# Optimization experiments

Measured on AMD Instinct MI355X. Metric: run time of the kernel, lower is better.

The kernel has to match this reference:

```python
import jax, jax.numpy as jnp
import numpy as np

N = 100000      # nodes per graph batch
E = 1600000     # edges
G = 64          # graphs (segments for GraphNorm)
F_IN = 128
F = 128         # hidden features
H = 4           # attention heads
C = F // H      # per-head channels
F_OUT = 64
N_GAT = 2       # layers - 2
EPS = 1e-5


def _add_self_loops(src, dst, n):
    loop = jnp.arange(n, dtype=src.dtype)
    return jnp.concatenate([src, loop]), jnp.concatenate([dst, loop])


def gcn_conv(x, src, dst, W, b, n):
    # PyG GCNConv: self-loops + symmetric deg^-1/2 normalization, add-aggr
    src, dst = _add_self_loops(src, dst, n)
    deg = jax.ops.segment_sum(jnp.ones(src.shape, x.dtype), dst, num_segments=n)
    dis = jnp.where(deg > 0, jax.lax.rsqrt(deg), 0.0)
    norm = dis[src] * dis[dst]                      # [E+N]
    h = x @ W.T                                     # [N,F]
    return jax.ops.segment_sum(h[src] * norm[:, None], dst, num_segments=n) + b


def graph_norm(x, batch, gamma, beta, alpha, g):
    # PyG GraphNorm: x_c = x - alpha*mean_g; out = gamma*x_c/sqrt(var_g+eps)+beta
    cnt = jnp.maximum(jax.ops.segment_sum(jnp.ones((x.shape[0],), x.dtype), batch, num_segments=g), 1.0)[:, None]
    mean = jax.ops.segment_sum(x, batch, num_segments=g) / cnt
    xc = x - alpha * mean[batch]
    var = jax.ops.segment_sum(xc * xc, batch, num_segments=g) / cnt
    return gamma * xc / jnp.sqrt(var[batch] + EPS) + beta


def gat_conv(x, src, dst, W, att_src, att_dst, b, n):
    # PyG GATConv (shared src/dst lin, self-loops, LeakyReLU(0.2), segment softmax)
    h = (x @ W.T).reshape(n, H, C)                  # [N,H,C]
    a_s = (h * att_src).sum(-1)                     # [N,H]
    a_d = (h * att_dst).sum(-1)                     # [N,H]
    src, dst = _add_self_loops(src, dst, n)
    e = jax.nn.leaky_relu(a_s[src] + a_d[dst], 0.2) # [E+N,H]
    emax = jax.ops.segment_max(e, dst, num_segments=n)
    ex = jnp.exp(e - emax[dst])
    den = jax.ops.segment_sum(ex, dst, num_segments=n)
    alpha = ex / (den[dst] + 1e-16)                 # [E+N,H]
    out = jax.ops.segment_sum(h[src] * alpha[:, :, None], dst, num_segments=n)
    return out.reshape(n, H * C) + b


def _branch(x, src, dst, batch, W0, b0, gn0_gamma, gn0_beta, gn0_alpha,
            gat_W, gat_att_src, gat_att_dst, gat_b, gn_gamma, gn_beta, gn_alpha,
            lin_W, lin_b):
    x = gcn_conv(x, src, dst, W0, b0, N)
    x = graph_norm(x, batch, gn0_gamma, gn0_beta, gn0_alpha, G)
    for i in range(N_GAT):
        h = gat_conv(x, src, dst, gat_W[i], gat_att_src[i], gat_att_dst[i], gat_b[i], N)
        h = jax.nn.gelu(h, approximate=False)
        x = x + graph_norm(h, batch, gn_gamma[i], gn_beta[i], gn_alpha[i], G)
    return x @ lin_W.T + lin_b


def setup_inputs() -> dict:
    key = jax.random.key(0)
    ks = jax.random.split(key, 16)
    inp = {
        'x1': jax.random.normal(ks[0], (N, F_IN), jnp.float32),
        'x2': jax.random.normal(ks[1], (N, F_IN), jnp.float32),
        'edge_index1': jax.random.randint(ks[2], (2, E), 0, N, jnp.int32),
        'edge_index2': jax.random.randint(ks[3], (2, E), 0, N, jnp.int32),
        'batch1': jnp.sort(jax.random.randint(ks[4], (N,), 0, G, jnp.int32)),
        'batch2': jnp.sort(jax.random.randint(ks[5], (N,), 0, G, jnp.int32)),
        'W0': jax.random.normal(ks[6], (F, F_IN), jnp.float32) * 0.05,
        'b0': jnp.zeros((F,), jnp.float32),
        'gn0_gamma': jnp.ones((F,), jnp.float32),
        'gn0_beta': jnp.zeros((F,), jnp.float32),
        'gn0_alpha': jnp.ones((F,), jnp.float32),
        'gat_W': jax.random.normal(ks[7], (N_GAT, F, F), jnp.float32) * 0.05,
        'gat_att_src': jax.random.normal(ks[8], (N_GAT, H, C), jnp.float32) * 0.05,
        'gat_att_dst': jax.random.normal(ks[9], (N_GAT, H, C), jnp.float32) * 0.05,
        'gat_b': jnp.zeros((N_GAT, F), jnp.float32),
        'gn_gamma': jnp.ones((N_GAT, F), jnp.float32),
        'gn_beta': jnp.zeros((N_GAT, F), jnp.float32),
        'gn_alpha': jnp.ones((N_GAT, F), jnp.float32),
        'lin_W': jax.random.normal(ks[10], (F_OUT, F), jnp.float32) * 0.05,
        'lin_b': jnp.zeros((F_OUT,), jnp.float32),
    }
    return inp


def reference(x1, x2, edge_index1, edge_index2, batch1, batch2,
              W0, b0, gn0_gamma, gn0_beta, gn0_alpha,
              gat_W, gat_att_src, gat_att_dst, gat_b, gn_gamma, gn_beta, gn_alpha,
              lin_W, lin_b):
    params = (W0, b0, gn0_gamma, gn0_beta, gn0_alpha, gat_W, gat_att_src,
              gat_att_dst, gat_b, gn_gamma, gn_beta, gn_alpha, lin_W, lin_b)
    o1 = _branch(x1, edge_index1[0], edge_index1[1], batch1, *params)
    o2 = _branch(x2, edge_index2[0], edge_index2[1], batch2, *params)
    return jnp.stack([o1, o2])  # [2, N, F_OUT]
```

## Files before the change

### kernel.cpp

```cpp
#include <hip/hip_runtime.h>
#include <hip/hip_bf16.h>

#define NN 100000
#define EE 1600000
#define GB 64

typedef unsigned int u32;
typedef unsigned short u16;

typedef __attribute__((ext_vector_type(8))) short bf16x8;
typedef __attribute__((ext_vector_type(4))) float f32x4;

#define CDIV(a, b) (((a) + (b) - 1) / (b))
#define NSB CDIV(NN, 1024)
#define NBB CDIV(EE, 4096)

__device__ __forceinline__ float bf2f(u16 v) { return __uint_as_float(((u32)v) << 16); }
__device__ __forceinline__ u16 f2bf(float f) {
    u32 u = __float_as_uint(f);
    u32 r = (u + 0x7fffu + ((u >> 16) & 1u)) >> 16;
    return (u16)r;
}
__device__ __forceinline__ float lrelu(float v) { return fmaxf(v, 0.2f * v); }
__device__ __forceinline__ float gelu_f(float v) { return 0.5f * v * (1.f + erff(v * 0.70710678118654752f)); }
__device__ __forceinline__ float cexp(float v) { return __expf(fminf(v, 30.f)); }

__global__ __launch_bounds__(256) void k_zero_f(float* __restrict__ p, int n) {
    int i = blockIdx.x * 256 + threadIdx.x;
    if (i < n) p[i] = 0.f;
}
__global__ __launch_bounds__(256) void k_zero_i(int* __restrict__ p, int n) {
    int i = blockIdx.x * 256 + threadIdx.x;
    if (i < n) p[i] = 0;
}
__global__ __launch_bounds__(256) void k_f2bf_arr(const float* __restrict__ src, u16* __restrict__ dst, int n) {
    int i4 = (blockIdx.x * 256 + threadIdx.x) * 4;
    if (i4 >= n) return;
    float4 v = *(const float4*)(src + i4);
    *(ushort4*)(dst + i4) = make_ushort4(f2bf(v.x), f2bf(v.y), f2bf(v.z), f2bf(v.w));
}

__global__ void k_cnt2(const int* __restrict__ b0, const int* __restrict__ b1, float* __restrict__ cnt, int n) {
    int t = threadIdx.x;
    if (t >= 128) return;
    int graph = t >> 6, g = t & 63;
    const int* batch = graph ? b1 : b0;
    int lo = 0, hi = n;
    while (lo < hi) { int m = (lo + hi) >> 1; if (batch[m] <= g) lo = m + 1; else hi = m; }
    int ub_g = lo;
    int v = g - 1;
    lo = 0; hi = n;
    while (lo < hi) { int m = (lo + hi) >> 1; if (batch[m] <= v) lo = m + 1; else hi = m; }
    cnt[graph * GB + g] = (float)(ub_g - lo);
}

__global__ __launch_bounds__(256) void k_bincnt(const int* __restrict__ d0, const int* __restrict__ d1,
                                                int* __restrict__ bin_cnt) {
    __shared__ int lcnt[NSB];
    int g = blockIdx.x / NBB, blk = blockIdx.x % NBB;
    const int* dst = g ? d1 : d0;
    int t = threadIdx.x;
    for (int i = t; i < NSB; i += 256) lcnt[i] = 0;
    __syncthreads();
    int base = blk * 4096;
#pragma unroll
    for (int k = 0; k < 16; ++k) {
        int ei = base + k * 256 + t;
        if (ei < EE) {
            int d = dst[ei];
            if ((u32)d < (u32)NN) atomicAdd(&lcnt[d >> 10], 1);
        }
    }
    __syncthreads();
    for (int i = t; i < NSB; i += 256)
        if (lcnt[i]) atomicAdd(&bin_cnt[g * NSB + i], lcnt[i]);
}

__global__ __launch_bounds__(128) void k_binscan(const int* __restrict__ bin_cnt, int* __restrict__ bin_base,
                                                 int* __restrict__ bin_cur, int* __restrict__ ptr) {
    __shared__ int sh[128];
    int g = blockIdx.x;
    int t = threadIdx.x;
    int v = (t < NSB) ? bin_cnt[g * NSB + t] : 0;
    sh[t] = v;
    __syncthreads();
    for (int o = 1; o < 128; o <<= 1) {
        int x = (t >= o) ? sh[t - o] : 0;
        __syncthreads();
        sh[t] += x;
        __syncthreads();
    }
    if (t < NSB) {
        bin_base[g * (NSB + 1) + t] = sh[t] - v;
        bin_cur[g * NSB + t] = sh[t] - v;
    }
    if (t == NSB - 1) {
        bin_base[g * (NSB + 1) + NSB] = sh[t];
        ptr[g * (NN + 1) + NN] = sh[t];
    }
}

__global__ __launch_bounds__(256) void k_bin(const int* __restrict__ s0, const int* __restrict__ d0,
                                             const int* __restrict__ s1, const int* __restrict__ d1,
                                             int* __restrict__ bin_cur, int2* __restrict__ binbuf) {
    __shared__ int lcnt[NSB], lbase[NSB];
    int g = blockIdx.x / NBB, blk = blockIdx.x % NBB;
    const int* src = g ? s1 : s0;
    const int* dst = g ? d1 : d0;
    int* bc = bin_cur + g * NSB;
    int2* bb = binbuf + (size_t)g * EE;
    int t = threadIdx.x;
    int base = blk * 4096;
    for (int i = t; i < NSB; i += 256) lcnt[i] = 0;
    __syncthreads();
    int lidx[16];
#pragma unroll
    for (int k = 0; k < 16; ++k) {
        int ei = base + k * 256 + t;
        lidx[k] = -1;
        if (ei < EE) {
            int d = dst[ei];
            if ((u32)d < (u32)NN) lidx[k] = atomicAdd(&lcnt[d >> 10], 1);
        }
    }
    __syncthreads();
    for (int i = t; i < NSB; i += 256) lbase[i] = atomicAdd(&bc[i], lcnt[i]);
    __syncthreads();
#pragma unroll
    for (int k = 0; k < 16; ++k) {
        int ei = base + k * 256 + t;
        if (ei < EE && lidx[k] >= 0) {
            int s = src[ei], d = dst[ei];
            int pos = lbase[d >> 10] + lidx[k];
            if ((u32)pos < (u32)EE) bb[pos] = make_int2(s, d);
        }
    }
}

__global__ __launch_bounds__(256) void k_csr_bin(const int* __restrict__ bin_base, const int2* __restrict__ binbuf,
                                                 int* __restrict__ ptr, float* __restrict__ dis,
                                                 int* __restrict__ srcs) {
    __shared__ int lcnt[1024];
    __shared__ int lsum[256];
    int g = blockIdx.x / NSB, b = blockIdx.x % NSB;
    int t = threadIdx.x;
    const int2* bb = binbuf + (size_t)g * EE;
    int beg = bin_base[g * (NSB + 1) + b];
    int end = bin_base[g * (NSB + 1) + b + 1];
    if (beg < 0) beg = 0;
    if (end > EE) end = EE;
    for (int i = t; i < 1024; i += 256) lcnt[i] = 0;
    __syncthreads();
    for (int j = beg + t; j < end; j += 256)
        atomicAdd(&lcnt[bb[j].y & 1023], 1);
    __syncthreads();
    int c0 = lcnt[t * 4], c1 = lcnt[t * 4 + 1], c2 = lcnt[t * 4 + 2], c3 = lcnt[t * 4 + 3];
    int ls = c0 + c1 + c2 + c3;
    lsum[t] = ls;
    __syncthreads();
    for (int o = 1; o < 256; o <<= 1) {
        int x = (t >= o) ? lsum[t - o] : 0;
        __syncthreads();
        lsum[t] += x;
        __syncthreads();
    }
    int e0 = lsum[t] - ls;
    int e1 = e0 + c0, e2 = e1 + c1, e3 = e2 + c2;
    int node0 = (b << 10) + t * 4;
    int* ptr_g = ptr + g * (NN + 1);
    float* dis_g = dis + g * NN;
    if (node0 + 0 < NN) { ptr_g[node0 + 0] = beg + e0; dis_g[node0 + 0] = rsqrtf((float)(c0 + 1)); }
    if (node0 + 1 < NN) { ptr_g[node0 + 1] = beg + e1; dis_g[node0 + 1] = rsqrtf((float)(c1 + 1)); }
    if (node0 + 2 < NN) { ptr_g[node0 + 2] = beg + e2; dis_g[node0 + 2] = rsqrtf((float)(c2 + 1)); }
    if (node0 + 3 < NN) { ptr_g[node0 + 3] = beg + e3; dis_g[node0 + 3] = rsqrtf((float)(c3 + 1)); }
    lcnt[t * 4] = e0; lcnt[t * 4 + 1] = e1; lcnt[t * 4 + 2] = e2; lcnt[t * 4 + 3] = e3;
    __syncthreads();
    int* sg = srcs + (size_t)g * EE;
    for (int j = beg + t; j < end; j += 256) {
        int2 sd = bb[j];
        int pos = beg + atomicAdd(&lcnt[sd.y & 1023], 1);
        if ((u32)pos < (u32)EE) sg[pos] = sd.x;
    }
}

template <int NC, bool XF32, bool FINAL>
__global__ __launch_bounds__(256) void k_gemm(const void* __restrict__ Xv, const u16* __restrict__ Wb,
                                              const float* __restrict__ bias, u16* __restrict__ Yb,
                                              float* __restrict__ Yf, int n) {
    constexpr int LD = 136;
    constexpr int HC = NC / 2;
    constexpr int NF = NC / 32;
    __shared__ __align__(16) u16 xs[64 * LD];
    __shared__ __align__(16) u16 wsh[NC * LD];
    const float* Xf = (const float*)Xv;
    const u16*   Xh = (const u16*)Xv;
    int t = threadIdx.x;
    int rowbase = blockIdx.x * 64;
    for (int i = t * 8; i < NC * 128; i += 2048) {
        int c = i >> 7, k = i & 127;
        *(bf16x8*)&wsh[c * LD + k] = *(const bf16x8*)(Wb + i);
    }
    if (XF32) {
        for (int i = t * 4; i < 64 * 128; i += 1024) {
            int r = i >> 7, k = i & 127;
            int row = rowbase + r;
            ushort4 xv = make_ushort4(0, 0, 0, 0);
            if (row < n) {
                float4 f = *(const float4*)(Xf + (size_t)row * 128 + k);
                xv = make_ushort4(f2bf(f.x), f2bf(f.y), f2bf(f.z), f2bf(f.w));
            }
            *(ushort4*)&xs[r * LD + k] = xv;
        }
    } else {
        for (int i = t * 8; i < 64 * 128; i += 2048) {
            int r = i >> 7, k = i & 127;
            int row = rowbase + r;
            bf16x8 xv = {0, 0, 0, 0, 0, 0, 0, 0};
            if (row < n) xv = *(const bf16x8*)(Xh + (size_t)row * 128 + k);
            *(bf16x8*)&xs[r * LD + k] = xv;
        }
    }
    __syncthreads();

    int lane = t & 63, wid = t >> 6;
    int rw = wid >> 1, cw = wid & 1;
    int l16 = lane & 15, kg = lane >> 4;

    f32x4 acc[2][NF];
#pragma unroll
    for (int m = 0; m < 2; ++m)
#pragma unroll
        for (int nf = 0; nf < NF; ++nf) acc[m][nf] = (f32x4){0.f, 0.f, 0.f, 0.f};

    const u16* ap0 = &xs[(rw * 32 + l16) * LD + kg * 8];
    const u16* bp0 = &wsh[(cw * HC + l16) * LD + kg * 8];
#pragma unroll
    for (int ks = 0; ks < 4; ++ks) {
        int k0 = ks * 32;
        bf16x8 a0 = *(const bf16x8*)(ap0 + k0);
        bf16x8 a1 = *(const bf16x8*)(ap0 + 16 * LD + k0);
        bf16x8 bfr[NF];
#pragma unroll
        for (int nf = 0; nf < NF; ++nf)
            bfr[nf] = *(const bf16x8*)(bp0 + nf * 16 * LD + k0);
#pragma unroll
        for (int nf = 0; nf < NF; ++nf) {
            acc[0][nf] = __builtin_amdgcn_mfma_f32_16x16x32_bf16(a0, bfr[nf], acc[0][nf], 0, 0, 0);
            acc[1][nf] = __builtin_amdgcn_mfma_f32_16x16x32_bf16(a1, bfr[nf], acc[1][nf], 0, 0, 0);
        }
    }

#pragma unroll
    for (int m = 0; m < 2; ++m) {
        int rloc = rw * 32 + m * 16 + kg * 4;
#pragma unroll
        for (int nf = 0; nf < NF; ++nf) {
            int col = cw * HC + nf * 16 + l16;
#pragma unroll
            for (int j = 0; j < 4; ++j) {
                int row = rowbase + rloc + j;
                if (row < n) {
                    if (FINAL) Yf[(size_t)row * NC + col] = acc[m][nf][j] + bias[col];
                    else       Yb[(size_t)row * NC + col] = f2bf(acc[m][nf][j]);
                }
            }
        }
    }
}

__global__ __launch_bounds__(256) void k_gcn_gather(const int* __restrict__ ptr, const int* __restrict__ srcs,
                                                    const float* __restrict__ dis, const u16* __restrict__ h,
                                                    const float* __restrict__ bias, u16* __restrict__ agg) {
    int tid = blockIdx.x * 256 + threadIdx.x;
    int node = tid >> 6, lane = tid & 63;
    if (node >= NN) return;
    int eg = lane >> 3, fl = lane & 7, f0 = fl * 16;
    float dd = dis[node];
    float acc[16];
    if (eg == 0) {
        bf16x8 h0 = *(const bf16x8*)(h + (size_t)node * 128 + f0);
        bf16x8 h1 = *(const bf16x8*)(h + (size_t)node * 128 + f0 + 8);
#pragma unroll
        for (int k = 0; k < 8; ++k) { acc[k] = bf2f((u16)h0[k]) * dd; acc[8 + k] = bf2f((u16)h1[k]) * dd; }
    } else {
#pragma unroll
        for (int k = 0; k < 16; ++k) acc[k] = 0.f;
    }
    int jb = ptr[node], je = ptr[node + 1];
    if (jb < 0) jb = 0;
    if (je > EE) je = EE;
    int j = jb + eg;
    for (; j + 8 < je; j += 16) {
        int s0 = srcs[j], s1 = srcs[j + 8];
        float d0 = dis[s0], d1 = dis[s1];
        bf16x8 a0 = *(const bf16x8*)(h + (size_t)s0 * 128 + f0);
        bf16x8 a1 = *(const bf16x8*)(h + (size_t)s0 * 128 + f0 + 8);
        bf16x8 b0 = *(const bf16x8*)(h + (size_t)s1 * 128 + f0);
        bf16x8 b1 = *(const bf16x8*)(h + (size_t)s1 * 128 + f0 + 8);
#pragma unroll
        for (int k = 0; k < 8; ++k) {
            acc[k]     += bf2f((u16)a0[k]) * d0 + bf2f((u16)b0[k]) * d1;
            acc[8 + k] += bf2f((u16)a1[k]) * d0 + bf2f((u16)b1[k]) * d1;
        }
    }
    for (; j < je; j += 8) {
        int s = srcs[j];
        float ds = dis[s];
        bf16x8 a0 = *(const bf16x8*)(h + (size_t)s * 128 + f0);
        bf16x8 a1 = *(const bf16x8*)(h + (size_t)s * 128 + f0 + 8);
#pragma unroll
        for (int k = 0; k < 8; ++k) {
            acc[k]     += bf2f((u16)a0[k]) * ds;
            acc[8 + k] += bf2f((u16)a1[k]) * ds;
        }
    }
#pragma unroll
    for (int k = 0; k < 16; ++k) {
        acc[k] += __shfl_xor(acc[k], 8);
        acc[k] += __shfl_xor(acc[k], 16);
        acc[k] += __shfl_xor(acc[k], 32);
    }
    if (eg == 0) {
        u16 o[16];
#pragma unroll
        for (int k = 0; k < 16; ++k) o[k] = f2bf(bias[f0 + k] + acc[k] * dd);
        *(bf16x8*)(agg + (size_t)node * 128 + f0)     = *(bf16x8*)&o[0];
        *(bf16x8*)(agg + (size_t)node * 128 + f0 + 8) = *(bf16x8*)&o[8];
    }
}

__global__ __launch_bounds__(256) void k_att(const u16* __restrict__ h, const float* __restrict__ aw_s,
                                             const float* __restrict__ aw_d, float* __restrict__ a_s,
                                             float* __restrict__ a_d, int n) {
    int i = blockIdx.x * 256 + threadIdx.x;
    if (i >= n * 4) return;
    int node = i >> 2, hd = i & 3;
    const u16* hp = h + (size_t)node * 128 + hd * 32;
    float s = 0.f, d = 0.f;
#pragma unroll
    for (int c0 = 0; c0 < 32; c0 += 4) {
        ushort4 hv = *(const ushort4*)(hp + c0);
        float h0 = bf2f(hv.x), h1 = bf2f(hv.y), h2 = bf2f(hv.z), h3 = bf2f(hv.w);
        const float* as_p = aw_s + hd * 32 + c0;
        const float* ad_p = aw_d + hd * 32 + c0;
        s += h0 * as_p[0] + h1 * as_p[1] + h2 * as_p[2] + h3 * as_p[3];
        d += h0 * ad_p[0] + h1 * ad_p[1] + h2 * ad_p[2] + h3 * ad_p[3];
    }
    a_s[i] = s;
    a_d[i] = d;
}

__global__ __launch_bounds__(256) void k_gat_gather(const int* __restrict__ ptr, const int* __restrict__ srcs,
                                                    const float* __restrict__ a_s, const float* __restrict__ a_d,
                                                    const u16* __restrict__ h,
                                                    const float* __restrict__ bias, u16* __restrict__ agg) {
    int tid = blockIdx.x * 256 + threadIdx.x;
    int node = tid >> 6, lane = tid & 63;
    if (node >= NN) return;
    int eg = lane >> 3, fl = lane & 7, f0 = fl * 16, hd = fl >> 1;
    float ad = a_d[node * 4 + hd];
    float acc[16];
    float den;
    if (eg == 0) {
        float exs = cexp(lrelu(a_s[node * 4 + hd] + ad));
        bf16x8 h0 = *(const bf16x8*)(h + (size_t)node * 128 + f0);
        bf16x8 h1 = *(const bf16x8*)(h + (size_t)node * 128 + f0 + 8);
#pragma unroll
        for (int k = 0; k < 8; ++k) { acc[k] = bf2f((u16)h0[k]) * exs; acc[8 + k] = bf2f((u16)h1[k]) * exs; }
        den = exs;
    } else {
#pragma unroll
        for (int k = 0; k < 16; ++k) acc[k] = 0.f;
        den = 0.f;
    }
    int jb = ptr[node], je = ptr[node + 1];
    if (jb < 0) jb = 0;
    if (je > EE) je = EE;
    int j = jb + eg;
    for (; j + 8 < je; j += 16) {
        int s0 = srcs[j], s1 = srcs[j + 8];
        float l0 = a_s[s0 * 4 + hd], l1 = a_s[s1 * 4 + hd];
        bf16x8 a0 = *(const bf16x8*)(h + (size_t)s0 * 128 + f0);
        bf16x8 a1 = *(const bf16x8*)(h + (size_t)s0 * 128 + f0 + 8);
        bf16x8 b0 = *(const bf16x8*)(h + (size_t)s1 * 128 + f0);
        bf16x8 b1 = *(const bf16x8*)(h + (size_t)s1 * 128 + f0 + 8);
        float ex0 = cexp(lrelu(l0 + ad));
        float ex1 = cexp(lrelu(l1 + ad));
#pragma unroll
        for (int k = 0; k < 8; ++k) {
            acc[k]     += bf2f((u16)a0[k]) * ex0 + bf2f((u16)b0[k]) * ex1;
            acc[8 + k] += bf2f((u16)a1[k]) * ex0 + bf2f((u16)b1[k]) * ex1;
        }
        den += ex0 + ex1;
    }
    for (; j < je; j += 8) {
        int s = srcs[j];
        float ex = cexp(lrelu(a_s[s * 4 + hd] + ad));
        bf16x8 a0 = *(const bf16x8*)(h + (size_t)s * 128 + f0);
        bf16x8 a1 = *(const bf16x8*)(h + (size_t)s * 128 + f0 + 8);
#pragma unroll
        for (int k = 0; k < 8; ++k) {
            acc[k]     += bf2f((u16)a0[k]) * ex;
            acc[8 + k] += bf2f((u16)a1[k]) * ex;
        }
        den += ex;
    }
#pragma unroll
    for (int k = 0; k < 16; ++k) {
        acc[k] += __shfl_xor(acc[k], 8);
        acc[k] += __shfl_xor(acc[k], 16);
        acc[k] += __shfl_xor(acc[k], 32);
    }
    den += __shfl_xor(den, 8);
    den += __shfl_xor(den, 16);
    den += __shfl_xor(den, 32);
    if (eg == 0) {
        float rdn = 1.f / (den + 1e-16f);
        u16 o[16];
#pragma unroll
        for (int k = 0; k < 16; ++k) o[k] = f2bf(bias[f0 + k] + acc[k] * rdn);
        *(bf16x8*)(agg + (size_t)node * 128 + f0)     = *(bf16x8*)&o[0];
        *(bf16x8*)(agg + (size_t)node * 128 + f0 + 8) = *(bf16x8*)&o[8];
    }
}

template <bool GELU>
__global__ __launch_bounds__(128) void k_gn_stats(const u16* __restrict__ X, const int* __restrict__ batch,
                                                  float* __restrict__ ssum, float* __restrict__ ssum2, int n) {
    int f = threadIdx.x;
    int base = blockIdx.x * 64;
    if (base >= n) return;
    int end = base + 64; if (end > n) end = n;
    float s1 = 0.f, s2 = 0.f;
    int curg = batch[base];
    if ((u32)curg >= (u32)GB) curg = 0;
    for (int node = base; node < end; ++node) {
        int g = batch[node];
        if ((u32)g >= (u32)GB) g = 0;
        if (g != curg) {
            atomicAdd(&ssum[curg * 128 + f], s1);
            atomicAdd(&ssum2[curg * 128 + f], s2);
            s1 = 0.f; s2 = 0.f; curg = g;
        }
        float v = bf2f(X[(size_t)node * 128 + f]);
        if (GELU) v = gelu_f(v);
        s1 += v; s2 += v * v;
    }
    atomicAdd(&ssum[curg * 128 + f], s1);
    atomicAdd(&ssum2[curg * 128 + f], s2);
}

__global__ __launch_bounds__(256) void k_gn_params(float* __restrict__ ssum, float* __restrict__ ssum2,
                                                   const float* __restrict__ cnt, const float* __restrict__ alpha,
                                                   const float* __restrict__ gamma, const float* __restrict__ beta) {
    int i = blockIdx.x * 256 + threadIdx.x;
    if (i >= GB * 128) return;
    int g = i >> 7, f = i & 127;
    float c = cnt[g]; if (!(c >= 1.f)) c = 1.f;
    float mu = ssum[i] / c;
    float m2 = ssum2[i] / c;
    float sh = alpha[f] * mu;
    float var = m2 - 2.f * sh * mu + sh * sh;
    var = fmaxf(var, 0.f);
    float inv = rsqrtf(var + 1e-5f);
    float A = gamma[f] * inv;
    ssum[i] = A;
    ssum2[i] = beta[f] - A * sh;
}

template <bool RESID, bool GELU>
__global__ __launch_bounds__(256) void k_gn_apply(const u16* __restrict__ X, const int* __restrict__ batch,
                                                  const float* __restrict__ A, const float* __restrict__ B,
                                                  u16* __restrict__ out, int n) {
    int i = blockIdx.x * 256 + threadIdx.x;
    if (i >= n * 32) return;
    int node = i >> 5, f0 = (i & 31) * 4;
    int g = batch[node];
    if ((u32)g >= (u32)GB) g = 0;
    ushort4 x = *(const ushort4*)(X + (size_t)node * 128 + f0);
    float4 a4 = *(const float4*)(A + g * 128 + f0);
    float4 b4 = *(const float4*)(B + g * 128 + f0);
    float v0 = bf2f(x.x), v1 = bf2f(x.y), v2 = bf2f(x.z), v3 = bf2f(x.w);
    if (GELU) { v0 = gelu_f(v0); v1 = gelu_f(v1); v2 = gelu_f(v2); v3 = gelu_f(v3); }
    float o0 = a4.x * v0 + b4.x;
    float o1 = a4.y * v1 + b4.y;
    float o2 = a4.z * v2 + b4.z;
    float o3 = a4.w * v3 + b4.w;
    u16* op = out + (size_t)node * 128 + f0;
    if (RESID) {
        ushort4 prev = *(const ushort4*)op;
        o0 += bf2f(prev.x); o1 += bf2f(prev.y); o2 += bf2f(prev.z); o3 += bf2f(prev.w);
    }
    *(ushort4*)op = make_ushort4(f2bf(o0), f2bf(o1), f2bf(o2), f2bf(o3));
}

extern "C" void kernel_launch(void* const* d_in, const int* in_sizes, int n_in,
                              void* d_out, int out_size, void* d_ws, size_t ws_size,
                              hipStream_t stream) {
    const float* x_in[2]   = {(const float*)d_in[0], (const float*)d_in[1]};
    const int*   ei[2]     = {(const int*)d_in[2], (const int*)d_in[3]};
    const int*   batch[2]  = {(const int*)d_in[4], (const int*)d_in[5]};
    const float* W0        = (const float*)d_in[6];
    const float* b0        = (const float*)d_in[7];
    const float* gn0_gamma = (const float*)d_in[8];
    const float* gn0_beta  = (const float*)d_in[9];
    const float* gn0_alpha = (const float*)d_in[10];
    const float* gat_W     = (const float*)d_in[11];
    const float* att_s     = (const float*)d_in[12];
    const float* att_d     = (const float*)d_in[13];
    const float* gat_b     = (const float*)d_in[14];
    const float* gn_gamma  = (const float*)d_in[15];
    const float* gn_beta   = (const float*)d_in[16];
    const float* gn_alpha  = (const float*)d_in[17];
    const float* lin_W     = (const float*)d_in[18];
    const float* lin_b     = (const float*)d_in[19];
    float* out = (float*)d_out;

    char* base = (char*)d_ws;
    size_t off = 0;
    auto alloc = [&](size_t bytes) { char* p = base + off; off += (bytes + 15) & ~(size_t)15; return p; };
    u16*   xcur  = (u16*)alloc((size_t)NN * 128 * 2);
    u16*   h_b   = (u16*)alloc((size_t)NN * 128 * 2);
    u16*   agg_b = (u16*)alloc((size_t)NN * 128 * 2);
    int*   ptr   = (int*)alloc((size_t)2 * (NN + 1) * 4);
    int*   srcs  = (int*)alloc((size_t)2 * EE * 4);
    float* dis   = (float*)alloc((size_t)2 * NN * 4);
    float* a_s   = (float*)alloc((size_t)NN * 4 * 4);
    float* a_d   = (float*)alloc((size_t)NN * 4 * 4);
    float* ssum  = (float*)alloc((size_t)GB * 128 * 4);
    float* ssum2 = (float*)alloc((size_t)GB * 128 * 4);
    float* cnt   = (float*)alloc((size_t)2 * GB * 4);
    int*   bin_cnt  = (int*)alloc((size_t)2 * NSB * 4);
    int*   bin_base = (int*)alloc((size_t)2 * (NSB + 1) * 4);
    int*   bin_cur  = (int*)alloc((size_t)2 * NSB * 4);
    u16*   wbuf  = (u16*)alloc((size_t)57344 * 2);
    int2*  binbuf = (int2*)xcur;

    if (ws_size < off) return;

    k_f2bf_arr<<<CDIV(16384 / 4, 256), 256, 0, stream>>>(W0, wbuf, 16384);
    k_f2bf_arr<<<CDIV(32768 / 4, 256), 256, 0, stream>>>(gat_W, wbuf + 16384, 32768);
    k_f2bf_arr<<<CDIV(8192 / 4, 256), 256, 0, stream>>>(lin_W, wbuf + 49152, 8192);

    k_cnt2<<<1, 128, 0, stream>>>(batch[0], batch[1], cnt, NN);
    k_zero_i<<<1, 256, 0, stream>>>(bin_cnt, 2 * NSB);
    k_bincnt<<<2 * NBB, 256, 0, stream>>>(ei[0] + EE, ei[1] + EE, bin_cnt);
    k_binscan<<<2, 128, 0, stream>>>(bin_cnt, bin_base, bin_cur, ptr);
    k_bin<<<2 * NBB, 256, 0, stream>>>(ei[0], ei[0] + EE, ei[1], ei[1] + EE, bin_cur, binbuf);
    k_csr_bin<<<2 * NSB, 256, 0, stream>>>(bin_base, binbuf, ptr, dis, srcs);

    for (int b = 0; b < 2; ++b) {
        const int*   bt     = batch[b];
        const int*   ptr_g  = ptr + b * (NN + 1);
        const int*   srcs_g = srcs + (size_t)b * EE;
        const float* dis_g  = dis + b * NN;
        const float* cnt_g  = cnt + b * GB;

        k_gemm<128, true, false><<<CDIV(NN, 64), 256, 0, stream>>>(
            x_in[b], wbuf, nullptr, h_b, nullptr, NN);
        k_gcn_gather<<<CDIV(NN * 64, 256), 256, 0, stream>>>(ptr_g, srcs_g, dis_g, h_b, b0, agg_b);
        k_zero_f<<<CDIV(2 * GB * 128, 256), 256, 0, stream>>>(ssum, 2 * GB * 128);
        k_gn_stats<false><<<CDIV(NN, 64), 128, 0, stream>>>(agg_b, bt, ssum, ssum2, NN);
        k_gn_params<<<CDIV(GB * 128, 256), 256, 0, stream>>>(ssum, ssum2, cnt_g, gn0_alpha, gn0_gamma, gn0_beta);
        k_gn_apply<false, false><<<CDIV(NN * 32, 256), 256, 0, stream>>>(agg_b, bt, ssum, ssum2, xcur, NN);

        for (int L = 0; L < 2; ++L) {
            const u16*   Wl  = wbuf + 16384 + (size_t)L * 16384;
            const float* asw = att_s + L * 128;
            const float* adw = att_d + L * 128;
            const float* bl  = gat_b + L * 128;
            k_gemm<128, false, false><<<CDIV(NN, 64), 256, 0, stream>>>(
                xcur, Wl, nullptr, h_b, nullptr, NN);
            k_att<<<CDIV(NN * 4, 256), 256, 0, stream>>>(h_b, asw, adw, a_s, a_d, NN);
            k_gat_gather<<<CDIV(NN * 64, 256), 256, 0, stream>>>(ptr_g, srcs_g, a_s, a_d, h_b, bl, agg_b);
            k_zero_f<<<CDIV(2 * GB * 128, 256), 256, 0, stream>>>(ssum, 2 * GB * 128);
            k_gn_stats<true><<<CDIV(NN, 64), 128, 0, stream>>>(agg_b, bt, ssum, ssum2, NN);
            k_gn_params<<<CDIV(GB * 128, 256), 256, 0, stream>>>(ssum, ssum2, cnt_g, gn_alpha + L * 128, gn_gamma + L * 128, gn_beta + L * 128);
            k_gn_apply<true, true><<<CDIV(NN * 32, 256), 256, 0, stream>>>(agg_b, bt, ssum, ssum2, xcur, NN);
        }

        k_gemm<64, false, true><<<CDIV(NN, 64), 256, 0, stream>>>(
            xcur, wbuf + 49152, lin_b, nullptr, out + (size_t)b * NN * 64, NN);
    }
}
```

Measured before the change: 1.244 ms.

## Restructure GraphNorm stats as per-graph segmented reduction with vectorized loads

GraphNorm statistics now use precomputed graph start offsets, assuming the batch array is sorted. Each graph is split across 8 blocks that read 8 bf16 features per thread with 16-byte loads, reduce through shuffles and shared memory, and issue a single atomic per feature. The previous version used one thread per feature walking 64 nodes serially with 2-byte loads. The params kernel now writes the A and B coefficients to separate buffers and clears the sum buffers for the next layer, which removes the per-layer zero-fill launches. This relies on batch being sorted and contiguous per graph.

```diff
diff --git a/kernel.cpp b/kernel.cpp
--- a/kernel.cpp
+++ b/kernel.cpp
@@ -40,7 +40,8 @@
     *(ushort4*)(dst + i4) = make_ushort4(f2bf(v.x), f2bf(v.y), f2bf(v.z), f2bf(v.w));
 }
 
-__global__ void k_cnt2(const int* __restrict__ b0, const int* __restrict__ b1, float* __restrict__ cnt, int n) {
+__global__ void k_cnt2(const int* __restrict__ b0, const int* __restrict__ b1,
+                       float* __restrict__ cnt, int* __restrict__ gstart, int n) {
     int t = threadIdx.x;
     if (t >= 128) return;
     int graph = t >> 6, g = t & 63;
@@ -52,6 +53,7 @@
     lo = 0; hi = n;
     while (lo < hi) { int m = (lo + hi) >> 1; if (batch[m] <= v) lo = m + 1; else hi = m; }
     cnt[graph * GB + g] = (float)(ub_g - lo);
+    gstart[graph * GB + g] = lo;
 }
 
 __global__ __launch_bounds__(256) void k_bincnt(const int* __restrict__ d0, const int* __restrict__ d1,
@@ -425,34 +427,50 @@
 }
 
 template <bool GELU>
-__global__ __launch_bounds__(128) void k_gn_stats(const u16* __restrict__ X, const int* __restrict__ batch,
-                                                  float* __restrict__ ssum, float* __restrict__ ssum2, int n) {
-    int f = threadIdx.x;
-    int base = blockIdx.x * 64;
-    if (base >= n) return;
-    int end = base + 64; if (end > n) end = n;
-    float s1 = 0.f, s2 = 0.f;
-    int curg = batch[base];
-    if ((u32)curg >= (u32)GB) curg = 0;
-    for (int node = base; node < end; ++node) {
-        int g = batch[node];
-        if ((u32)g >= (u32)GB) g = 0;
-        if (g != curg) {
-            atomicAdd(&ssum[curg * 128 + f], s1);
-            atomicAdd(&ssum2[curg * 128 + f], s2);
-            s1 = 0.f; s2 = 0.f; curg = g;
-        }
-        float v = bf2f(X[(size_t)node * 128 + f]);
-        if (GELU) v = gelu_f(v);
-        s1 += v; s2 += v * v;
-    }
-    atomicAdd(&ssum[curg * 128 + f], s1);
-    atomicAdd(&ssum2[curg * 128 + f], s2);
+__global__ __launch_bounds__(256) void k_gn_stats(const u16* __restrict__ X, const int* __restrict__ gstart,
+                                                  const float* __restrict__ cnt,
+                                                  float* __restrict__ ssum, float* __restrict__ ssum2) {
+    __shared__ float red[4][16][16];
+    int g = blockIdx.x >> 3, c = blockIdx.x & 7;
+    int t = threadIdx.x;
+    int fg = t & 15, rp = t >> 4;
+    int gs = gstart[g];
+    int sz = (int)cnt[g];
+    int r0 = gs + (int)(((long long)sz * c) >> 3);
+    int r1 = gs + (int)(((long long)sz * (c + 1)) >> 3);
+    float s1[8], s2[8];
+#pragma unroll
+    for (int k = 0; k < 8; ++k) { s1[k] = 0.f; s2[k] = 0.f; }
+    for (int r = r0 + rp; r < r1; r += 16) {
+        bf16x8 v = *(const bf16x8*)(X + (size_t)r * 128 + fg * 8);
+#pragma unroll
+        for (int k = 0; k < 8; ++k) {
+            float f = bf2f((u16)v[k]);
+            if (GELU) f = gelu_f(f);
+            s1[k] += f; s2[k] += f * f;
+        }
+    }
+#pragma unroll
+    for (int k = 0; k < 8; ++k) {
+        s1[k] += __shfl_xor(s1[k], 16); s1[k] += __shfl_xor(s1[k], 32);
+        s2[k] += __shfl_xor(s2[k], 16); s2[k] += __shfl_xor(s2[k], 32);
+    }
+    if (((t >> 4) & 3) == 0) {
+#pragma unroll
+        for (int k = 0; k < 8; ++k) { red[t >> 6][fg][k] = s1[k]; red[t >> 6][fg][8 + k] = s2[k]; }
+    }
+    __syncthreads();
+    int fg2 = t >> 4, idx = t & 15;
+    float v = red[0][fg2][idx] + red[1][fg2][idx] + red[2][fg2][idx] + red[3][fg2][idx];
+    int f = fg2 * 8 + (idx & 7);
+    float* dstp = (idx < 8) ? &ssum[g * 128 + f] : &ssum2[g * 128 + f];
+    atomicAdd(dstp, v);
 }
 
 __global__ __launch_bounds__(256) void k_gn_params(float* __restrict__ ssum, float* __restrict__ ssum2,
                                                    const float* __restrict__ cnt, const float* __restrict__ alpha,
-                                                   const float* __restrict__ gamma, const float* __restrict__ beta) {
+                                                   const float* __restrict__ gamma, const float* __restrict__ beta,
+                                                   float* __restrict__ A, float* __restrict__ B) {
     int i = blockIdx.x * 256 + threadIdx.x;
     if (i >= GB * 128) return;
     int g = i >> 7, f = i & 127;
@@ -463,9 +481,11 @@
     float var = m2 - 2.f * sh * mu + sh * sh;
     var = fmaxf(var, 0.f);
     float inv = rsqrtf(var + 1e-5f);
-    float A = gamma[f] * inv;
-    ssum[i] = A;
-    ssum2[i] = beta[f] - A * sh;
+    float gA = gamma[f] * inv;
+    A[i] = gA;
+    B[i] = beta[f] - gA * sh;
+    ssum[i] = 0.f;
+    ssum2[i] = 0.f;
 }
 
 template <bool RESID, bool GELU>
@@ -529,7 +549,10 @@
     float* a_d   = (float*)alloc((size_t)NN * 4 * 4);
     float* ssum  = (float*)alloc((size_t)GB * 128 * 4);
     float* ssum2 = (float*)alloc((size_t)GB * 128 * 4);
+    float* abuf  = (float*)alloc((size_t)GB * 128 * 4);
+    float* bbuf  = (float*)alloc((size_t)GB * 128 * 4);
     float* cnt   = (float*)alloc((size_t)2 * GB * 4);
+    int*   gstart = (int*)alloc((size_t)2 * GB * 4);
     int*   bin_cnt  = (int*)alloc((size_t)2 * NSB * 4);
     int*   bin_base = (int*)alloc((size_t)2 * (NSB + 1) * 4);
     int*   bin_cur  = (int*)alloc((size_t)2 * NSB * 4);
@@ -541,8 +564,9 @@
     k_f2bf_arr<<<CDIV(16384 / 4, 256), 256, 0, stream>>>(W0, wbuf, 16384);
     k_f2bf_arr<<<CDIV(32768 / 4, 256), 256, 0, stream>>>(gat_W, wbuf + 16384, 32768);
     k_f2bf_arr<<<CDIV(8192 / 4, 256), 256, 0, stream>>>(lin_W, wbuf + 49152, 8192);
-
-    k_cnt2<<<1, 128, 0, stream>>>(batch[0], batch[1], cnt, NN);
+    k_zero_f<<<CDIV(2 * GB * 128, 256), 256, 0, stream>>>(ssum, 2 * GB * 128);
+
+    k_cnt2<<<1, 128, 0, stream>>>(batch[0], batch[1], cnt, gstart, NN);
     k_zero_i<<<1, 256, 0, stream>>>(bin_cnt, 2 * NSB);
     k_bincnt<<<2 * NBB, 256, 0, stream>>>(ei[0] + EE, ei[1] + EE, bin_cnt);
     k_binscan<<<2, 128, 0, stream>>>(bin_cnt, bin_base, bin_cur, ptr);
@@ -550,19 +574,19 @@
     k_csr_bin<<<2 * NSB, 256, 0, stream>>>(bin_base, binbuf, ptr, dis, srcs);
 
     for (int b = 0; b < 2; ++b) {
-        const int*   bt     = batch[b];
-        const int*   ptr_g  = ptr + b * (NN + 1);
-        const int*   srcs_g = srcs + (size_t)b * EE;
-        const float* dis_g  = dis + b * NN;
-        const float* cnt_g  = cnt + b * GB;
+        const int*   bt      = batch[b];
+        const int*   ptr_g   = ptr + b * (NN + 1);
+        const int*   srcs_g  = srcs + (size_t)b * EE;
+        const float* dis_g   = dis + b * NN;
+        const float* cnt_g   = cnt + b * GB;
+        const int*   gstart_g = gstart + b * GB;
 
         k_gemm<128, true, false><<<CDIV(NN, 64), 256, 0, stream>>>(
             x_in[b], wbuf, nullptr, h_b, nullptr, NN);
         k_gcn_gather<<<CDIV(NN * 64, 256), 256, 0, stream>>>(ptr_g, srcs_g, dis_g, h_b, b0, agg_b);
-        k_zero_f<<<CDIV(2 * GB * 128, 256), 256, 0, stream>>>(ssum, 2 * GB * 128);
-        k_gn_stats<false><<<CDIV(NN, 64), 128, 0, stream>>>(agg_b, bt, ssum, ssum2, NN);
-        k_gn_params<<<CDIV(GB * 128, 256), 256, 0, stream>>>(ssum, ssum2, cnt_g, gn0_alpha, gn0_gamma, gn0_beta);
-        k_gn_apply<false, false><<<CDIV(NN * 32, 256), 256, 0, stream>>>(agg_b, bt, ssum, ssum2, xcur, NN);
+        k_gn_stats<false><<<GB * 8, 256, 0, stream>>>(agg_b, gstart_g, cnt_g, ssum, ssum2);
+        k_gn_params<<<CDIV(GB * 128, 256), 256, 0, stream>>>(ssum, ssum2, cnt_g, gn0_alpha, gn0_gamma, gn0_beta, abuf, bbuf);
+        k_gn_apply<false, false><<<CDIV(NN * 32, 256), 256, 0, stream>>>(agg_b, bt, abuf, bbuf, xcur, NN);
 
         for (int L = 0; L < 2; ++L) {
             const u16*   Wl  = wbuf + 16384 + (size_t)L * 16384;
@@ -573,10 +597,9 @@
                 xcur, Wl, nullptr, h_b, nullptr, NN);
             k_att<<<CDIV(NN * 4, 256), 256, 0, stream>>>(h_b, asw, adw, a_s, a_d, NN);
             k_gat_gather<<<CDIV(NN * 64, 256), 256, 0, stream>>>(ptr_g, srcs_g, a_s, a_d, h_b, bl, agg_b);
-            k_zero_f<<<CDIV(2 * GB * 128, 256), 256, 0, stream>>>(ssum, 2 * GB * 128);
-            k_gn_stats<true><<<CDIV(NN, 64), 128, 0, stream>>>(agg_b, bt, ssum, ssum2, NN);
-            k_gn_params<<<CDIV(GB * 128, 256), 256, 0, stream>>>(ssum, ssum2, cnt_g, gn_alpha + L * 128, gn_gamma + L * 128, gn_beta + L * 128);
-            k_gn_apply<true, true><<<CDIV(NN * 32, 256), 256, 0, stream>>>(agg_b, bt, ssum, ssum2, xcur, NN);
+            k_gn_stats<true><<<GB * 8, 256, 0, stream>>>(agg_b, gstart_g, cnt_g, ssum, ssum2);
+            k_gn_params<<<CDIV(GB * 128, 256), 256, 0, stream>>>(ssum, ssum2, cnt_g, gn_alpha + L * 128, gn_gamma + L * 128, gn_beta + L * 128, abuf, bbuf);
+            k_gn_apply<true, true><<<CDIV(NN * 32, 256), 256, 0, stream>>>(agg_b, bt, abuf, bbuf, xcur, NN);
         }
 
         k_gemm<64, false, true><<<CDIV(NN, 64), 256, 0, stream>>>(
```

After: 1.139 ms. -8.5%, faster.
